# Performance work log

Measured on AMD Instinct MI355X. Metric: run time of the kernel, lower is better.

## Reference

```python
import jax, jax.numpy as jnp
import numpy as np

N_NODES = 100_000
DEG = 16
N_EDGES = N_NODES * DEG
NODE_F = 128
EDGE_F = 16
HID = 64
B = 64
K = DEG


def setup_inputs() -> dict:
    key = jax.random.key(0)
    ks = jax.random.split(key, 12)
    # node i's outgoing edges are at ids i + k*N_NODES for k in [0, DEG)
    src = jnp.arange(N_EDGES, dtype=jnp.int32) % N_NODES
    dst = jax.random.randint(ks[0], (N_EDGES,), 0, N_NODES, dtype=jnp.int32)
    edge_index = jnp.stack([src, dst])
    current_nodes = jax.random.randint(ks[1], (B,), 0, N_NODES, dtype=jnp.int32)
    # reachable neighbors = destinations of the current node's real edges
    neighbor_nodes = dst[current_nodes[:, None] + jnp.arange(K, dtype=jnp.int32)[None, :] * N_NODES]
    x = jax.random.normal(ks[2], (N_NODES, NODE_F), jnp.float32)
    edge_attr = jax.random.normal(ks[3], (N_EDGES, EDGE_F), jnp.float32)
    return dict(
        x=x,
        edge_attr=edge_attr,
        conv1_W=jax.random.normal(ks[4], (NODE_F, HID), jnp.float32) * (NODE_F ** -0.5),
        conv1_b=jnp.zeros((HID,), jnp.float32),
        conv2_W=jax.random.normal(ks[5], (HID, HID), jnp.float32) * (HID ** -0.5),
        conv2_b=jnp.zeros((HID,), jnp.float32),
        mlp_W1=jax.random.normal(ks[6], (2 * HID + EDGE_F, 2 * HID), jnp.float32) * ((2 * HID + EDGE_F) ** -0.5),
        mlp_b1=jnp.zeros((2 * HID,), jnp.float32),
        mlp_W2=jax.random.normal(ks[7], (2 * HID, 1), jnp.float32) * ((2 * HID) ** -0.5),
        mlp_b2=jnp.zeros((1,), jnp.float32),
        edge_index=edge_index,
        current_nodes=current_nodes,
        neighbor_nodes=neighbor_nodes,
    )


def gcn_conv(x, edge_index, W, b):
    """PyG GCNConv: symmetric norm with self-loops, then linear + bias."""
    n = x.shape[0]
    loop = jnp.arange(n, dtype=edge_index.dtype)
    src = jnp.concatenate([edge_index[0], loop])  # messages flow src -> dst
    dst = jnp.concatenate([edge_index[1], loop])
    xw = x @ W                                    # [N, H]
    deg = jnp.zeros((n,), xw.dtype).at[dst].add(1.0)
    dinv = jnp.where(deg > 0, jax.lax.rsqrt(deg), 0.0)
    msg = (dinv[src] * dinv[dst])[:, None] * xw[src]      # [E+N, H]
    return jax.ops.segment_sum(msg, dst, num_segments=n) + b


def reference(x, edge_attr, conv1_W, conv1_b, conv2_W, conv2_b,
              mlp_W1, mlp_b1, mlp_W2, mlp_b2,
              edge_index, current_nodes, neighbor_nodes):
    n = x.shape[0]
    h = jax.nn.relu(gcn_conv(x, edge_index, conv1_W, conv1_b))
    h = jax.nn.relu(gcn_conv(h, edge_index, conv2_W, conv2_b))

    # First edge id matching each (current, neighbor) pair, replacing the
    # original O(E)-per-neighbor boolean-mask loop with a sorted-key lookup.
    keys = edge_index[0].astype(jnp.int64) * n + edge_index[1].astype(jnp.int64)
    order = jnp.argsort(keys, stable=True)        # stable -> leftmost == first edge id
    skeys = keys[order]
    query = current_nodes[:, None].astype(jnp.int64) * n + neighbor_nodes.astype(jnp.int64)
    pos = jnp.clip(jnp.searchsorted(skeys, query), 0, skeys.shape[0] - 1)
    valid = skeys[pos] == query                   # [B, K]
    eid = order[pos]
    ea = edge_attr[eid]                           # [B, K, F]

    b_, k_ = neighbor_nodes.shape
    h_cur = jnp.broadcast_to(h[current_nodes][:, None, :], (b_, k_, h.shape[1]))
    h_nbr = h[neighbor_nodes]
    m = jnp.concatenate([h_cur, h_nbr, ea], axis=-1)  # [B, K, 2H+F]
    q = (jax.nn.relu(m @ mlp_W1 + mlp_b1) @ mlp_W2 + mlp_b2)[..., 0]
    q = jnp.where(valid, q, 0.0)
    return q, valid
```

## Files before the change

kernel.cpp:

```cpp
#include <hip/hip_runtime.h>

#define N_NODES 100000
#define DEG 16
#define N_EDGES (N_NODES * DEG)
#define NODE_F 128
#define EDGE_F 16
#define HID 64
#define NQ 1024
#define NCHUNK (N_EDGES / 256)
#define NHIST 2048
#define XT32 (N_NODES / 32)
#define TOTAL_A (NHIST + XT32)
#define BCAP 56
#define NDINV ((N_NODES + 255) / 256)
#define MAGIC 0x13579BDF

__device__ __forceinline__ int xcc_id() {
  int x;
  asm("s_getreg_b32 %0, hwreg(HW_REG_XCC_ID)" : "=s"(x));
  return x & 7;
}

__global__ void k_query_zero(const int* __restrict__ dst, const int* __restrict__ cur,
                             const int* __restrict__ nbr, int* __restrict__ n1,
                             int* __restrict__ n2, int* __restrict__ wcur,
                             int* __restrict__ eid_sel, float* __restrict__ out_valid,
                             int* __restrict__ degp) {
  if (blockIdx.x >= 4) {
    int4* d4 = (int4*)degp;
    const int n4 = 8 * N_NODES / 4;
    int i = (blockIdx.x - 4) * 256 + threadIdx.x;
    const int stride = (gridDim.x - 4) * 256;
    for (; i < n4; i += stride) d4[i] = make_int4(0, 0, 0, 0);
    return;
  }
  int i = blockIdx.x * 256 + threadIdx.x;
  if (i >= NQ) return;
  int b = i >> 4;
  int c = cur[b];
  int nb = nbr[i];
  int sel = -1;
  #pragma unroll
  for (int j = 0; j < DEG; ++j) {
    int e = c + j * N_NODES;
    if (sel < 0 && dst[e] == nb) sel = e;
  }
  eid_sel[i] = sel;
  out_valid[i] = (sel >= 0) ? 1.0f : 0.0f;
  n2[c] = MAGIC; n2[nb] = MAGIC;
  n1[c] = MAGIC; n1[nb] = MAGIC;
  wcur[c] = 0;   wcur[nb] = 0;
}

__global__ __launch_bounds__(256) void k_fusedA(
    const float* __restrict__ x, const float* __restrict__ Wg,
    float* __restrict__ xw, const int* __restrict__ dst,
    const int* __restrict__ n2, int* __restrict__ n1, int* __restrict__ wcur,
    int* __restrict__ degp) {
  __shared__ float xs[32 * 128];
  const int t = threadIdx.x;
  const int bid = blockIdx.x;

  const int h0 = (int)(((long)bid * NHIST) / TOTAL_A);
  const int h1b = (int)(((long)(bid + 1) * NHIST) / TOTAL_A);

  if (h1b > h0) {
    int* __restrict__ dp = degp + (size_t)xcc_id() * N_NODES;
    const int stride = NHIST * 256;
    for (int e = h0 * 256 + t; e < N_EDGES; e += stride) {
      int d = dst[e];
      __hip_atomic_fetch_add(&dp[d], 1, __ATOMIC_RELAXED,
                             __HIP_MEMORY_SCOPE_WORKGROUP);
      if (n2[d] == MAGIC) {
        int s = e % N_NODES;
        n1[s] = MAGIC;
        wcur[s] = 0;
      }
    }
    return;
  }

  const long base = (long)(bid - h0) * 32;

  const float4* __restrict__ xv = (const float4*)x;
  #pragma unroll
  for (int p = 0; p < 4; ++p) {
    int f4 = p * 256 + t;
    int r = f4 >> 5;
    int c4 = f4 & 31;
    float4 v = xv[(base + r) * 32 + c4];
    float* xr = xs + r * 128;
    xr[((c4 << 2) + 0) ^ r] = v.x;
    xr[((c4 << 2) + 1) ^ r] = v.y;
    xr[((c4 << 2) + 2) ^ r] = v.z;
    xr[((c4 << 2) + 3) ^ r] = v.w;
  }
  __syncthreads();

  float acc[8];
  #pragma unroll
  for (int j = 0; j < 8; ++j) acc[j] = 0.f;
  const int r = t & 31;
  const int cg = t >> 5;
  const float* __restrict__ xrow = xs + r * 128;
  const float4* __restrict__ wp = (const float4*)(Wg + cg * 8);
  #pragma unroll 4
  for (int k = 0; k < NODE_F; ++k) {
    float xk = xrow[k ^ r];
    float4 w0 = wp[k * 16 + 0];
    float4 w1 = wp[k * 16 + 1];
    acc[0] = fmaf(xk, w0.x, acc[0]); acc[1] = fmaf(xk, w0.y, acc[1]);
    acc[2] = fmaf(xk, w0.z, acc[2]); acc[3] = fmaf(xk, w0.w, acc[3]);
    acc[4] = fmaf(xk, w1.x, acc[4]); acc[5] = fmaf(xk, w1.y, acc[5]);
    acc[6] = fmaf(xk, w1.z, acc[6]); acc[7] = fmaf(xk, w1.w, acc[7]);
  }
  long gr = base + r;
  float4* __restrict__ op = (float4*)(xw + gr * HID + cg * 8);
  op[0] = make_float4(acc[0], acc[1], acc[2], acc[3]);
  op[1] = make_float4(acc[4], acc[5], acc[6], acc[7]);
}

__global__ void k_bucket_dinv(const int* __restrict__ dst, const int* __restrict__ n1,
                              int* __restrict__ wcur, int* __restrict__ bucket,
                              const int* __restrict__ degp, float* __restrict__ dinv) {
  if (blockIdx.x < NDINV) {
    int v = blockIdx.x * 256 + threadIdx.x;
    if (v < N_NODES) {
      int s = 1;
      #pragma unroll
      for (int p = 0; p < 8; ++p) s += degp[(size_t)p * N_NODES + v];
      dinv[v] = rsqrtf((float)s);
    }
    return;
  }
  int e = (blockIdx.x - NDINV) * 256 + threadIdx.x;
  int d = dst[e];
  if (n1[d] != MAGIC) return;
  int pos = atomicAdd(&wcur[d], 1);
  if (pos >= 0 && pos < BCAP)
    bucket[(size_t)d * BCAP + pos] = e % N_NODES;
}

__global__ __launch_bounds__(256) void k_gather_xw2(
    const int* __restrict__ bucket, const int* __restrict__ wcur,
    const int* __restrict__ n1, const float* __restrict__ dinv,
    const float* __restrict__ xw, const float* __restrict__ bias,
    const float* __restrict__ W2g, float* __restrict__ xw2) {
  const int t = threadIdx.x;
  const int lane = t & 63;
  const int v = blockIdx.x * 4 + (t >> 6);
  if (v >= N_NODES) return;
  if (n1[v] != MAGIC) return;
  int n = wcur[v];
  if (n > BCAP) n = BCAP;
  if (n < 0) n = 0;
  int   s_l = (lane < n) ? bucket[(size_t)v * BCAP + lane] : 0;
  float w_l = (lane < n) ? dinv[s_l] : 0.f;
  float acc = 0.f;
  int j = 0;
  for (; j + 3 < n; j += 4) {
    int s0 = __shfl(s_l, j);
    int s1 = __shfl(s_l, j + 1);
    int s2 = __shfl(s_l, j + 2);
    int s3 = __shfl(s_l, j + 3);
    float a0 = xw[(size_t)s0 * HID + lane];
    float a1 = xw[(size_t)s1 * HID + lane];
    float a2 = xw[(size_t)s2 * HID + lane];
    float a3 = xw[(size_t)s3 * HID + lane];
    acc = fmaf(__shfl(w_l, j), a0, acc);
    acc = fmaf(__shfl(w_l, j + 1), a1, acc);
    acc = fmaf(__shfl(w_l, j + 2), a2, acc);
    acc = fmaf(__shfl(w_l, j + 3), a3, acc);
  }
  for (; j < n; ++j)
    acc = fmaf(__shfl(w_l, j), xw[(size_t)__shfl(s_l, j) * HID + lane], acc);
  float dv = dinv[v];
  acc = fmaf(dv, xw[(size_t)v * HID + lane], acc);
  float h = fmaxf(fmaf(dv, acc, bias[lane]), 0.f);
  float a2s = 0.f;
  #pragma unroll
  for (int f = 0; f < HID; ++f)
    a2s = fmaf(__shfl(h, f), W2g[f * HID + lane], a2s);
  xw2[(size_t)v * HID + lane] = a2s;
}

__global__ __launch_bounds__(256) void k_gather(
    const int* __restrict__ bucket, const int* __restrict__ wcur,
    const int* __restrict__ flag, const float* __restrict__ dinv,
    const float* __restrict__ xw, const float* __restrict__ bias,
    float* __restrict__ hout) {
  const int t = threadIdx.x;
  const int lane = t & 63;
  const int v = blockIdx.x * 4 + (t >> 6);
  if (v >= N_NODES) return;
  if (flag[v] != MAGIC) return;
  int n = wcur[v];
  if (n > BCAP) n = BCAP;
  if (n < 0) n = 0;
  int   s_l = (lane < n) ? bucket[(size_t)v * BCAP + lane] : 0;
  float w_l = (lane < n) ? dinv[s_l] : 0.f;
  float acc = 0.f;
  int j = 0;
  for (; j + 3 < n; j += 4) {
    int s0 = __shfl(s_l, j);
    int s1 = __shfl(s_l, j + 1);
    int s2 = __shfl(s_l, j + 2);
    int s3 = __shfl(s_l, j + 3);
    float a0 = xw[(size_t)s0 * HID + lane];
    float a1 = xw[(size_t)s1 * HID + lane];
    float a2 = xw[(size_t)s2 * HID + lane];
    float a3 = xw[(size_t)s3 * HID + lane];
    acc = fmaf(__shfl(w_l, j), a0, acc);
    acc = fmaf(__shfl(w_l, j + 1), a1, acc);
    acc = fmaf(__shfl(w_l, j + 2), a2, acc);
    acc = fmaf(__shfl(w_l, j + 3), a3, acc);
  }
  for (; j < n; ++j)
    acc = fmaf(__shfl(w_l, j), xw[(size_t)__shfl(s_l, j) * HID + lane], acc);
  float dv = dinv[v];
  acc = fmaf(dv, xw[(size_t)v * HID + lane], acc);
  hout[(size_t)v * HID + lane] = fmaxf(fmaf(dv, acc, bias[lane]), 0.f);
}

__global__ void k_mlp(const float* __restrict__ h2, const float* __restrict__ ea,
                      const float* __restrict__ W1, const float* __restrict__ b1,
                      const float* __restrict__ W2, const float* __restrict__ b2,
                      const int* __restrict__ cur, const int* __restrict__ nbr,
                      const int* __restrict__ eid_sel, float* __restrict__ out) {
  __shared__ float m[2 * HID + EDGE_F];
  __shared__ float red[128];
  const int q = blockIdx.x;
  const int t = threadIdx.x;
  const int eid = eid_sel[q];
  if (eid < 0) {
    if (t == 0) out[q] = 0.0f;
    return;
  }
  const int b = q >> 4;
  const int c = cur[b];
  const int nb = nbr[q];
  if (t < HID)    m[t] = h2[(size_t)c * HID + t];
  else            m[t] = h2[(size_t)nb * HID + (t - HID)];
  if (t < EDGE_F) m[2 * HID + t] = ea[(size_t)eid * EDGE_F + t];
  __syncthreads();
  float h = b1[t];
  #pragma unroll
  for (int j = 0; j < 2 * HID + EDGE_F; ++j) h = fmaf(m[j], W1[j * 128 + t], h);
  h = fmaxf(h, 0.f) * W2[t];
  red[t] = h;
  __syncthreads();
  if (t < 64) {
    float v = red[t] + red[t + 64];
    #pragma unroll
    for (int o = 32; o > 0; o >>= 1) v += __shfl_down(v, o);
    if (t == 0) out[q] = v + b2[0];
  }
}

extern "C" void kernel_launch(void* const* d_in, const int* in_sizes, int n_in,
                              void* d_out, int out_size, void* d_ws, size_t ws_size,
                              hipStream_t stream) {
  const float* x    = (const float*)d_in[0];
  const float* ea   = (const float*)d_in[1];
  const float* c1W  = (const float*)d_in[2];
  const float* c1b  = (const float*)d_in[3];
  const float* c2W  = (const float*)d_in[4];
  const float* c2b  = (const float*)d_in[5];
  const float* mW1  = (const float*)d_in[6];
  const float* mb1  = (const float*)d_in[7];
  const float* mW2  = (const float*)d_in[8];
  const float* mb2  = (const float*)d_in[9];
  const int*   eidx = (const int*)d_in[10];
  const int*   cur  = (const int*)d_in[11];
  const int*   nbr  = (const int*)d_in[12];
  const int* edst = eidx + N_EDGES;
  float* out = (float*)d_out;

  char* p = (char*)d_ws;
  auto alloc = [&](size_t bytes) -> void* {
    void* r = (void*)p;
    p += (bytes + 255) & ~(size_t)255;
    return r;
  };
  int*   degp    = (int*)alloc((size_t)8 * N_NODES * 4);
  float* dinv    = (float*)alloc((size_t)N_NODES * 4);
  int*   n1      = (int*)alloc((size_t)N_NODES * 4);
  int*   n2      = (int*)alloc((size_t)N_NODES * 4);
  int*   wcur    = (int*)alloc((size_t)N_NODES * 4);
  int*   eid_sel = (int*)alloc((size_t)NQ * 4);
  int*   bucket  = (int*)alloc((size_t)N_NODES * BCAP * 4);
  float* xw1     = (float*)alloc((size_t)N_NODES * HID * 4);
  float* xw2     = (float*)alloc((size_t)N_NODES * HID * 4);
  float* h2      = xw1;

  k_query_zero<<<260, 256, 0, stream>>>(edst, cur, nbr, n1, n2, wcur, eid_sel,
                                        out + NQ, degp);
  k_fusedA<<<TOTAL_A, 256, 0, stream>>>(x, c1W, xw1, edst, n2, n1, wcur, degp);
  k_bucket_dinv<<<NDINV + NCHUNK, 256, 0, stream>>>(edst, n1, wcur, bucket, degp,
                                                    dinv);
  k_gather_xw2<<<(N_NODES + 3) / 4, 256, 0, stream>>>(bucket, wcur, n1, dinv, xw1,
                                                      c1b, c2W, xw2);
  k_gather<<<(N_NODES + 3) / 4, 256, 0, stream>>>(bucket, wcur, n2, dinv, xw2,
                                                  c2b, h2);
  k_mlp<<<NQ, 128, 0, stream>>>(h2, ea, mW1, mb1, mW2, mb2, cur, nbr, eid_sel, out);
}
```

Baseline: 385.8 us.

## Use 4x4 register tiles and 64-row blocks in fused x@W kernel

The GEMM part of the fused histogram/xw kernel now processes 64 rows per block instead of 32. Each thread computes a 4x4 output tile from float4 shared-memory reads with an XOR swizzle, in place of one row by 8 columns with scalar reads. This raises register-level reuse of both x and W and cuts shared-memory and global W loads per FMA. The interleaved assignment of histogram and GEMM blocks is replaced by a simple split where the first NHIST blocks do the histogram, and bounds checks are added for the partial final tile.

```diff
diff --git a/kernel.cpp b/kernel.cpp
--- a/kernel.cpp
+++ b/kernel.cpp
@@ -9,8 +9,8 @@
 #define NQ 1024
 #define NCHUNK (N_EDGES / 256)
 #define NHIST 2048
-#define XT32 (N_NODES / 32)
-#define TOTAL_A (NHIST + XT32)
+#define XT64 ((N_NODES + 63) / 64)
+#define TOTAL_A (NHIST + XT64)
 #define BCAP 56
 #define NDINV ((N_NODES + 255) / 256)
 #define MAGIC 0x13579BDF
@@ -57,17 +57,14 @@
     float* __restrict__ xw, const int* __restrict__ dst,
     const int* __restrict__ n2, int* __restrict__ n1, int* __restrict__ wcur,
     int* __restrict__ degp) {
-  __shared__ float xs[32 * 128];
+  __shared__ float4 xs4[64 * 32];
   const int t = threadIdx.x;
   const int bid = blockIdx.x;
 
-  const int h0 = (int)(((long)bid * NHIST) / TOTAL_A);
-  const int h1b = (int)(((long)(bid + 1) * NHIST) / TOTAL_A);
-
-  if (h1b > h0) {
+  if (bid < NHIST) {
     int* __restrict__ dp = degp + (size_t)xcc_id() * N_NODES;
     const int stride = NHIST * 256;
-    for (int e = h0 * 256 + t; e < N_EDGES; e += stride) {
+    for (int e = bid * 256 + t; e < N_EDGES; e += stride) {
       int d = dst[e];
       __hip_atomic_fetch_add(&dp[d], 1, __ATOMIC_RELAXED,
                              __HIP_MEMORY_SCOPE_WORKGROUP);
@@ -80,44 +77,73 @@
     return;
   }
 
-  const long base = (long)(bid - h0) * 32;
+  const long base = (long)(bid - NHIST) * 64;
 
   const float4* __restrict__ xv = (const float4*)x;
   #pragma unroll
-  for (int p = 0; p < 4; ++p) {
+  for (int p = 0; p < 8; ++p) {
     int f4 = p * 256 + t;
     int r = f4 >> 5;
-    int c4 = f4 & 31;
-    float4 v = xv[(base + r) * 32 + c4];
-    float* xr = xs + r * 128;
-    xr[((c4 << 2) + 0) ^ r] = v.x;
-    xr[((c4 << 2) + 1) ^ r] = v.y;
-    xr[((c4 << 2) + 2) ^ r] = v.z;
-    xr[((c4 << 2) + 3) ^ r] = v.w;
+    int k4 = f4 & 31;
+    long gr = base + r;
+    float4 v = (gr < N_NODES) ? xv[gr * 32 + k4]
+                              : make_float4(0.f, 0.f, 0.f, 0.f);
+    xs4[r * 32 + (k4 ^ ((r >> 2) & 7))] = v;
   }
   __syncthreads();
 
-  float acc[8];
-  #pragma unroll
-  for (int j = 0; j < 8; ++j) acc[j] = 0.f;
-  const int r = t & 31;
-  const int cg = t >> 5;
-  const float* __restrict__ xrow = xs + r * 128;
-  const float4* __restrict__ wp = (const float4*)(Wg + cg * 8);
-  #pragma unroll 4
-  for (int k = 0; k < NODE_F; ++k) {
-    float xk = xrow[k ^ r];
-    float4 w0 = wp[k * 16 + 0];
-    float4 w1 = wp[k * 16 + 1];
-    acc[0] = fmaf(xk, w0.x, acc[0]); acc[1] = fmaf(xk, w0.y, acc[1]);
-    acc[2] = fmaf(xk, w0.z, acc[2]); acc[3] = fmaf(xk, w0.w, acc[3]);
-    acc[4] = fmaf(xk, w1.x, acc[4]); acc[5] = fmaf(xk, w1.y, acc[5]);
-    acc[6] = fmaf(xk, w1.z, acc[6]); acc[7] = fmaf(xk, w1.w, acc[7]);
-  }
-  long gr = base + r;
-  float4* __restrict__ op = (float4*)(xw + gr * HID + cg * 8);
-  op[0] = make_float4(acc[0], acc[1], acc[2], acc[3]);
-  op[1] = make_float4(acc[4], acc[5], acc[6], acc[7]);
+  const int rg = (t >> 4) << 2;
+  const int cq = t & 15;
+  const float4* __restrict__ wq = (const float4*)Wg + cq;
+
+  float acc[4][4];
+  #pragma unroll
+  for (int i = 0; i < 4; ++i)
+    #pragma unroll
+    for (int j = 0; j < 4; ++j) acc[i][j] = 0.f;
+
+  const int sw = (rg >> 2) & 7;
+  for (int k4 = 0; k4 < 32; ++k4) {
+    float4 xf0 = xs4[(rg + 0) * 32 + (k4 ^ sw)];
+    float4 xf1 = xs4[(rg + 1) * 32 + (k4 ^ sw)];
+    float4 xf2 = xs4[(rg + 2) * 32 + (k4 ^ sw)];
+    float4 xf3 = xs4[(rg + 3) * 32 + (k4 ^ sw)];
+    float4 wf0 = wq[(k4 * 4 + 0) * 16];
+    float4 wf1 = wq[(k4 * 4 + 1) * 16];
+    float4 wf2 = wq[(k4 * 4 + 2) * 16];
+    float4 wf3 = wq[(k4 * 4 + 3) * 16];
+#define FMA_ROW(i, xf)                                                  \
+    acc[i][0] = fmaf(xf.x, wf0.x, acc[i][0]);                           \
+    acc[i][1] = fmaf(xf.x, wf0.y, acc[i][1]);                           \
+    acc[i][2] = fmaf(xf.x, wf0.z, acc[i][2]);                           \
+    acc[i][3] = fmaf(xf.x, wf0.w, acc[i][3]);                           \
+    acc[i][0] = fmaf(xf.y, wf1.x, acc[i][0]);                           \
+    acc[i][1] = fmaf(xf.y, wf1.y, acc[i][1]);                           \
+    acc[i][2] = fmaf(xf.y, wf1.z, acc[i][2]);                           \
+    acc[i][3] = fmaf(xf.y, wf1.w, acc[i][3]);                           \
+    acc[i][0] = fmaf(xf.z, wf2.x, acc[i][0]);                           \
+    acc[i][1] = fmaf(xf.z, wf2.y, acc[i][1]);                           \
+    acc[i][2] = fmaf(xf.z, wf2.z, acc[i][2]);                           \
+    acc[i][3] = fmaf(xf.z, wf2.w, acc[i][3]);                           \
+    acc[i][0] = fmaf(xf.w, wf3.x, acc[i][0]);                           \
+    acc[i][1] = fmaf(xf.w, wf3.y, acc[i][1]);                           \
+    acc[i][2] = fmaf(xf.w, wf3.z, acc[i][2]);                           \
+    acc[i][3] = fmaf(xf.w, wf3.w, acc[i][3]);
+    FMA_ROW(0, xf0)
+    FMA_ROW(1, xf1)
+    FMA_ROW(2, xf2)
+    FMA_ROW(3, xf3)
+#undef FMA_ROW
+  }
+
+  #pragma unroll
+  for (int i = 0; i < 4; ++i) {
+    long gr = base + rg + i;
+    if (gr < N_NODES) {
+      float4* __restrict__ op = (float4*)(xw + gr * HID);
+      op[cq] = make_float4(acc[i][0], acc[i][1], acc[i][2], acc[i][3]);
+    }
+  }
 }
 
 __global__ void k_bucket_dinv(const int* __restrict__ dst, const int* __restrict__ n1,
```

New measurement: 345.3 us. 1.12x faster.
